# Kernel optimization log

Hardware: AMD Instinct MI355X
Metric: run time of the kernel (lower is better)

Reference implementation:

```python
import jax, jax.numpy as jnp
import numpy as np

WIN = 7
K1, K2 = 0.01, 0.03


def _box_filter(x, w):
    """Valid-padding uniform box filter. x: (B, D, H, W); w: (1, 1, k, k)."""
    B, D, H, Wd = x.shape
    k = w.shape[-1]
    y = jax.lax.conv_general_dilated(
        x.reshape(B * D, 1, H, Wd), w, window_strides=(1, 1), padding='VALID',
        dimension_numbers=('NCHW', 'OIHW', 'NCHW'))
    return y.reshape(B, D, H - k + 1, Wd - k + 1)


def setup_inputs() -> dict:
    key = jax.random.key(0)
    kx, ky = jax.random.split(key)
    X = jax.random.uniform(kx, (4, 64, 256, 256), dtype=jnp.float32)
    Y = jax.random.uniform(ky, (4, 64, 256, 256), dtype=jnp.float32)
    w = jnp.ones((1, 1, WIN, WIN), dtype=jnp.float32) / (WIN * WIN)  # buffer self.w
    return {"X": X, "Y": Y, "w": w}


def reference(X, Y, w):
    data_range = 1.0
    C1 = (K1 * data_range) ** 2
    C2 = (K2 * data_range) ** 2
    NP = WIN * WIN
    cov_norm = NP / (NP - 1)

    ux = _box_filter(X, w)
    uy = _box_filter(Y, w)
    uxx = _box_filter(X * X, w)
    uyy = _box_filter(Y * Y, w)
    uxy = _box_filter(X * Y, w)

    vx = cov_norm * (uxx - ux * ux)
    vy = cov_norm * (uyy - uy * uy)
    vxy = cov_norm * (uxy - ux * uy)

    A1 = 2.0 * ux * uy + C1
    A2 = 2.0 * vxy + C2
    B1 = ux * ux + uy * uy + C1
    B2 = vx + vy + C2
    S = (A1 * A2) / (B1 * B2)  # (B, D, H', W')

    # Faithful to torch: ssim_per_slice[:, i] = S_i.mean() (mean over batch AND spatial),
    # then 1 - mean over depth, returned per batch element.
    slice_means = S.mean(axis=(0, 2, 3))  # (D,)
    loss = 1.0 - slice_means.mean()
    return jnp.full((X.shape[0],), loss, dtype=X.dtype)
```

## Files before the change

kernel.cpp:

```cpp
#include <hip/hip_runtime.h>

#define H 256
#define W 256
#define W4 (W / 4)
#define OWID 250
#define OHEI 250
#define NIMG 256
#define BAND 28
#define NBANDS 9
#define NBLK (NBANDS * NIMG)
#define VPAD 264

__device__ __forceinline__ float4 f4zero() { return make_float4(0.f, 0.f, 0.f, 0.f); }

__device__ __forceinline__ void vacc(float4& s, const float4 n, const float4 o) {
    s.x += n.x - o.x; s.y += n.y - o.y; s.z += n.z - o.z; s.w += n.w - o.w;
}
__device__ __forceinline__ void vaccp(float4& s, const float4 a, const float4 b,
                                      const float4 c, const float4 d) {
    s.x += a.x * b.x - c.x * d.x;
    s.y += a.y * b.y - c.y * d.y;
    s.z += a.z * b.z - c.z * d.z;
    s.w += a.w * b.w - c.w * d.w;
}

__global__ __launch_bounds__(64) void ssim_band_kernel(
    const float* __restrict__ X, const float* __restrict__ Y,
    float* __restrict__ partial)
{
    __shared__ float vsx[VPAD], vsy[VPAD], vsxx[VPAD], vsyy[VPAD], vsxy[VPAD];

    const int lane = threadIdx.x;
    const int band = blockIdx.x;
    const int img  = blockIdx.y;
    const int r0 = band * BAND;
    const int out_rows = (OHEI - r0 < BAND) ? (OHEI - r0) : BAND;
    const int rows_in = out_rows + 6;

    const float4* Xp = (const float4*)X + ((size_t)img * H + r0) * W4 + lane;
    const float4* Yp = (const float4*)Y + ((size_t)img * H + r0) * W4 + lane;

    float4 xh[7], yh[7];
    float4 sx = f4zero(), sy = f4zero(), sxx = f4zero(), syy = f4zero(), sxy = f4zero();

    #pragma unroll
    for (int i = 0; i < 6; ++i) {
        float4 xv = Xp[i * W4];
        float4 yv = Yp[i * W4];
        xh[i] = xv; yh[i] = yv;
        vacc(sx, xv, f4zero());
        vacc(sy, yv, f4zero());
        vaccp(sxx, xv, xv, f4zero(), f4zero());
        vaccp(syy, yv, yv, f4zero(), f4zero());
        vaccp(sxy, xv, yv, f4zero(), f4zero());
    }
    xh[6] = f4zero(); yh[6] = f4zero();

    float4 xn = Xp[6 * W4];
    float4 yn = Yp[6 * W4];

    const float inv_np   = 1.0f / 49.0f;
    const float cov_norm = 49.0f / 48.0f;
    const float C1 = 1e-4f;
    const float C2 = 9e-4f;
    float lsum = 0.0f;

    for (int base = 6; base < rows_in; base += 7) {
        #pragma unroll
        for (int i = 0; i < 7; ++i) {
            const int r = base + i;
            if (r < rows_in) {
                const int slot = (6 + i) % 7;
                float4 xf, yf;
                const bool more = (r + 1 < rows_in);
                if (more) { xf = Xp[(r + 1) * W4]; yf = Yp[(r + 1) * W4]; }

                const float4 xo = xh[slot], yo = yh[slot];
                vacc(sx, xn, xo);
                vacc(sy, yn, yo);
                vaccp(sxx, xn, xn, xo, xo);
                vaccp(syy, yn, yn, yo, yo);
                vaccp(sxy, xn, yn, xo, yo);
                xh[slot] = xn; yh[slot] = yn;

                ((float4*)vsx)[lane] = sx;
                ((float4*)vsy)[lane] = sy;
                ((float4*)vsxx)[lane] = sxx;
                ((float4*)vsyy)[lane] = syy;
                ((float4*)vsxy)[lane] = sxy;
                __syncthreads();

                float wx[4], wy[4], wxx[4], wyy[4], wxy[4];
                #define HWIN(VS, S, WA)                                        \
                {                                                              \
                    float4 b = ((const float4*)VS)[lane + 1];                  \
                    float2 c = *(const float2*)&VS[4 * lane + 8];              \
                    WA[0] = S.x + S.y + S.z + S.w + b.x + b.y + b.z;           \
                    WA[1] = WA[0] - S.x + b.w;                                 \
                    WA[2] = WA[1] - S.y + c.x;                                 \
                    WA[3] = WA[2] - S.z + c.y;                                 \
                }
                HWIN(vsx,  sx,  wx)
                HWIN(vsy,  sy,  wy)
                HWIN(vsxx, sxx, wxx)
                HWIN(vsyy, syy, wyy)
                HWIN(vsxy, sxy, wxy)
                #undef HWIN
                __syncthreads();

                #pragma unroll
                for (int s = 0; s < 4; ++s) {
                    float ux  = wx[s]  * inv_np;
                    float uy  = wy[s]  * inv_np;
                    float uxx = wxx[s] * inv_np;
                    float uyy = wyy[s] * inv_np;
                    float uxy = wxy[s] * inv_np;
                    float vx  = cov_norm * (uxx - ux * ux);
                    float vy  = cov_norm * (uyy - uy * uy);
                    float vxy = cov_norm * (uxy - ux * uy);
                    float A1 = 2.f * ux * uy + C1;
                    float A2 = 2.f * vxy + C2;
                    float B1 = ux * ux + uy * uy + C1;
                    float B2 = vx + vy + C2;
                    float S = (A1 * A2) * __builtin_amdgcn_rcpf(B1 * B2);
                    if (4 * lane + s < OWID) lsum += S;
                }
                xn = xf; yn = yf;
            }
        }
    }

    #pragma unroll
    for (int off = 32; off > 0; off >>= 1)
        lsum += __shfl_down(lsum, off, 64);
    if (lane == 0) partial[img * NBANDS + band] = lsum;
}

__global__ __launch_bounds__(256) void ssim_reduce_kernel(
    const float* __restrict__ partial, float* __restrict__ out)
{
    const int tid = threadIdx.x;
    double acc = 0.0;
    for (int i = tid; i < NBLK; i += 256)
        acc += (double)partial[i];
    #pragma unroll
    for (int off = 32; off > 0; off >>= 1)
        acc += __shfl_down(acc, off, 64);
    __shared__ double wsumd[4];
    if ((tid & 63) == 0) wsumd[tid >> 6] = acc;
    __syncthreads();
    if (tid == 0) {
        double total = wsumd[0] + wsumd[1] + wsumd[2] + wsumd[3];
        float loss = (float)(1.0 - total / 16000000.0);
        out[0] = loss; out[1] = loss; out[2] = loss; out[3] = loss;
    }
}

extern "C" void kernel_launch(void* const* d_in, const int* in_sizes, int n_in,
                              void* d_out, int out_size, void* d_ws, size_t ws_size,
                              hipStream_t stream) {
    const float* X = (const float*)d_in[0];
    const float* Y = (const float*)d_in[1];
    float* out = (float*)d_out;
    float* partial = (float*)d_ws;

    hipLaunchKernelGGL(ssim_band_kernel, dim3(NBANDS, NIMG), dim3(64), 0, stream,
                       X, Y, partial);
    hipLaunchKernelGGL(ssim_reduce_kernel, dim3(1), dim3(256), 0, stream,
                       partial, out);
}
```

Before: 160.0 us.

## Replace LDS horizontal window with wavefront shuffles and use smaller fully-unrolled bands

The horizontal 7-tap window sum now reads neighbour lanes' column sums through __shfl_down instead of writing them to shared memory, which removes two __syncthreads and the LDS round trip per row. Bands shrink from 28 to 10 rows (25 bands), so the row loop has a compile-time trip count and is fully unrolled, and launch bounds request higher occupancy. The SSIM arithmetic is rescaled to work on raw window sums with pre-scaled constants, which drops the per-value 1/49 multiplies. Smaller bands re-read 6 halo rows per band (about 60% extra global loads versus about 21% before), and the last band now reads past row 250 into rows that are loaded but not used.

```diff
diff --git a/kernel.cpp b/kernel.cpp
--- a/kernel.cpp
+++ b/kernel.cpp
@@ -4,12 +4,11 @@
 #define W 256
 #define W4 (W / 4)
 #define OWID 250
-#define OHEI 250
 #define NIMG 256
-#define BAND 28
-#define NBANDS 9
+#define BAND 10
+#define NBANDS 25
 #define NBLK (NBANDS * NIMG)
-#define VPAD 264
+#define ROWS_IN (BAND + 6)
 
 __device__ __forceinline__ float4 f4zero() { return make_float4(0.f, 0.f, 0.f, 0.f); }
 
@@ -24,18 +23,27 @@
     s.w += a.w * b.w - c.w * d.w;
 }
 
-__global__ __launch_bounds__(64) void ssim_band_kernel(
+#define HWIN(S, WA) do {                                        \
+    float bx = __shfl_down(S.x, 1);                             \
+    float by = __shfl_down(S.y, 1);                             \
+    float bz = __shfl_down(S.z, 1);                             \
+    float bw = __shfl_down(S.w, 1);                             \
+    float cx = __shfl_down(S.x, 2);                             \
+    float cy = __shfl_down(S.y, 2);                             \
+    WA[0] = ((S.x + S.y) + (S.z + S.w)) + ((bx + by) + bz);     \
+    WA[1] = WA[0] - S.x + bw;                                   \
+    WA[2] = WA[1] - S.y + cx;                                   \
+    WA[3] = WA[2] - S.z + cy;                                   \
+} while (0)
+
+__global__ __launch_bounds__(64, 4) void ssim_band_kernel(
     const float* __restrict__ X, const float* __restrict__ Y,
     float* __restrict__ partial)
 {
-    __shared__ float vsx[VPAD], vsy[VPAD], vsxx[VPAD], vsyy[VPAD], vsxy[VPAD];
-
     const int lane = threadIdx.x;
     const int band = blockIdx.x;
     const int img  = blockIdx.y;
     const int r0 = band * BAND;
-    const int out_rows = (OHEI - r0 < BAND) ? (OHEI - r0) : BAND;
-    const int rows_in = out_rows + 6;
 
     const float4* Xp = (const float4*)X + ((size_t)img * H + r0) * W4 + lane;
     const float4* Yp = (const float4*)Y + ((size_t)img * H + r0) * W4 + lane;
@@ -54,80 +62,53 @@
         vaccp(syy, yv, yv, f4zero(), f4zero());
         vaccp(sxy, xv, yv, f4zero(), f4zero());
     }
-    xh[6] = f4zero(); yh[6] = f4zero();
 
     float4 xn = Xp[6 * W4];
     float4 yn = Yp[6 * W4];
 
-    const float inv_np   = 1.0f / 49.0f;
-    const float cov_norm = 49.0f / 48.0f;
-    const float C1 = 1e-4f;
-    const float C2 = 9e-4f;
+    const float C1N  = 0.2401f;
+    const float C2N  = 2.1609f;
+    const float COV  = 49.0f / 48.0f;
+    const float COV2 = 2.0f * COV;
     float lsum = 0.0f;
 
-    for (int base = 6; base < rows_in; base += 7) {
+    #pragma unroll
+    for (int r = 6; r < ROWS_IN; ++r) {
+        float4 xf, yf;
+        if (r + 1 < ROWS_IN) {
+            xf = Xp[(r + 1) * W4];
+            yf = Yp[(r + 1) * W4];
+        }
+        const int slot = r % 7;
+        const float4 xo = xh[slot], yo = yh[slot];
+        vacc(sx, xn, xo);
+        vacc(sy, yn, yo);
+        vaccp(sxx, xn, xn, xo, xo);
+        vaccp(syy, yn, yn, yo, yo);
+        vaccp(sxy, xn, yn, xo, yo);
+        xh[slot] = xn; yh[slot] = yn;
+
+        float wx[4], wy[4], wxx[4], wyy[4], wxy[4];
+        HWIN(sx,  wx);
+        HWIN(sy,  wy);
+        HWIN(sxx, wxx);
+        HWIN(syy, wyy);
+        HWIN(sxy, wxy);
+
         #pragma unroll
-        for (int i = 0; i < 7; ++i) {
-            const int r = base + i;
-            if (r < rows_in) {
-                const int slot = (6 + i) % 7;
-                float4 xf, yf;
-                const bool more = (r + 1 < rows_in);
-                if (more) { xf = Xp[(r + 1) * W4]; yf = Yp[(r + 1) * W4]; }
-
-                const float4 xo = xh[slot], yo = yh[slot];
-                vacc(sx, xn, xo);
-                vacc(sy, yn, yo);
-                vaccp(sxx, xn, xn, xo, xo);
-                vaccp(syy, yn, yn, yo, yo);
-                vaccp(sxy, xn, yn, xo, yo);
-                xh[slot] = xn; yh[slot] = yn;
-
-                ((float4*)vsx)[lane] = sx;
-                ((float4*)vsy)[lane] = sy;
-                ((float4*)vsxx)[lane] = sxx;
-                ((float4*)vsyy)[lane] = syy;
-                ((float4*)vsxy)[lane] = sxy;
-                __syncthreads();
-
-                float wx[4], wy[4], wxx[4], wyy[4], wxy[4];
-                #define HWIN(VS, S, WA)                                        \
-                {                                                              \
-                    float4 b = ((const float4*)VS)[lane + 1];                  \
-                    float2 c = *(const float2*)&VS[4 * lane + 8];              \
-                    WA[0] = S.x + S.y + S.z + S.w + b.x + b.y + b.z;           \
-                    WA[1] = WA[0] - S.x + b.w;                                 \
-                    WA[2] = WA[1] - S.y + c.x;                                 \
-                    WA[3] = WA[2] - S.z + c.y;                                 \
-                }
-                HWIN(vsx,  sx,  wx)
-                HWIN(vsy,  sy,  wy)
-                HWIN(vsxx, sxx, wxx)
-                HWIN(vsyy, syy, wyy)
-                HWIN(vsxy, sxy, wxy)
-                #undef HWIN
-                __syncthreads();
-
-                #pragma unroll
-                for (int s = 0; s < 4; ++s) {
-                    float ux  = wx[s]  * inv_np;
-                    float uy  = wy[s]  * inv_np;
-                    float uxx = wxx[s] * inv_np;
-                    float uyy = wyy[s] * inv_np;
-                    float uxy = wxy[s] * inv_np;
-                    float vx  = cov_norm * (uxx - ux * ux);
-                    float vy  = cov_norm * (uyy - uy * uy);
-                    float vxy = cov_norm * (uxy - ux * uy);
-                    float A1 = 2.f * ux * uy + C1;
-                    float A2 = 2.f * vxy + C2;
-                    float B1 = ux * ux + uy * uy + C1;
-                    float B2 = vx + vy + C2;
-                    float S = (A1 * A2) * __builtin_amdgcn_rcpf(B1 * B2);
-                    if (4 * lane + s < OWID) lsum += S;
-                }
-                xn = xf; yn = yf;
-            }
+        for (int s = 0; s < 4; ++s) {
+            const float SX = wx[s], SY = wy[s];
+            const float t1 = SX * SY;
+            const float t2 = SX * SX;
+            const float t3 = SY * SY;
+            const float A1 = 2.0f * t1 + C1N;
+            const float B1 = (t2 + t3) + C1N;
+            const float A2 = COV2 * (49.0f * wxy[s] - t1) + C2N;
+            const float B2 = COV * (49.0f * (wxx[s] + wyy[s]) - (t2 + t3)) + C2N;
+            const float S = (A1 * A2) * __builtin_amdgcn_rcpf(B1 * B2);
+            if (4 * lane + s < OWID) lsum += S;
         }
+        xn = xf; yn = yf;
     }
 
     #pragma unroll
```

Result: slower. 198.6 us (+24.1%).
